# Kernel tuning notes

Hardware: AMD Instinct MI355X
Metric: run time of the kernel (lower is better)

The kernel has to match this reference:

```python
import jax, jax.numpy as jnp
import numpy as np

EPS = 1e-7
N_INST = 16  # instance ids 1..16 (id 0 = background); all present w.h.p. given input distribution


def setup_inputs() -> dict:
    key = jax.random.key(0)
    k1, k2, k3 = jax.random.split(key, 3)
    pred_instance_mask = jax.random.uniform(k1, (4, 17, 768, 768), dtype=jnp.float32)
    cls_out = jax.random.uniform(k2, (4, 1, 768, 768), dtype=jnp.float32)
    target_mask = jax.random.randint(k3, (4, 1, 768, 768), 0, 17, dtype=jnp.int32)
    return {"pred_instance_mask": pred_instance_mask, "cls_out": cls_out, "target_mask": target_mask}


def _bce_dice(p, t):
    # BCEDiceLoss(activation=None): mean BCE on probabilities + soft-dice loss
    pc = jnp.clip(p, EPS, 1.0 - EPS)
    bce = -jnp.mean(t * jnp.log(pc) + (1.0 - t) * jnp.log1p(-pc))
    inter = jnp.sum(p * t)
    dice = 1.0 - (2.0 * inter + EPS) / (jnp.sum(p) + jnp.sum(t) + EPS)
    return bce + dice


def reference(pred_instance_mask, cls_out, target_mask):
    B, K, H, W = pred_instance_mask.shape
    tfg = (target_mask > 0).astype(jnp.float32)
    res = _bce_dice(cls_out, tfg)
    res = res + _bce_dice(pred_instance_mask[:, 0:1], 1.0 - tfg)

    # ---- pairwise BCEDice loss matrix L[n, k] for ids n=1..N_INST, channels k=1..K-1 ----
    # Each pairwise loss is over the FULL tensor (all B*H*W pixels), target = (target_mask == n).
    Pm = pred_instance_mask[:, 1:].transpose(1, 0, 2, 3).reshape(K - 1, -1)  # [K-1, M]
    Mpix = Pm.shape[1]
    tm = target_mask.reshape(-1)  # [M] int ids
    pc = jnp.clip(Pm, EPS, 1.0 - EPS)
    log1mp = jnp.log1p(-pc)
    D = log1mp - jnp.log(pc)  # [K-1, M]; BCE = mean(-log1mp) + mean(t * D)
    A = -jnp.mean(log1mp, axis=1)  # [K-1]
    segD = jax.ops.segment_sum(D.T, tm, num_segments=N_INST + 1)[1:]   # [N, K-1]
    segP = jax.ops.segment_sum(Pm.T, tm, num_segments=N_INST + 1)[1:]  # [N, K-1] = inter
    cnt = jax.ops.segment_sum(jnp.ones_like(tm, dtype=jnp.float32), tm, num_segments=N_INST + 1)[1:]  # [N]
    sum_p = jnp.sum(Pm, axis=1)  # [K-1]
    bce = A[None, :] + segD / jnp.float32(Mpix)
    dice = 1.0 - (2.0 * segP + EPS) / (sum_p[None, :] + cnt[:, None] + EPS)
    L = bce + dice  # [N, K-1]

    # ---- greedy assignment: ids in ascending order each grab the remaining best channel ----
    def step(carry, Ln):
        avail, total = carry
        masked = jnp.where(avail, Ln, jnp.inf)
        k = jnp.argmin(masked)
        return (avail.at[k].set(False), total + masked[k]), None

    (_, total), _ = jax.lax.scan(step, (jnp.ones(K - 1, dtype=bool), jnp.float32(0.0)), L)
    return (res + total) / N_INST
```

## Files before the change

### kernel.cpp

```cpp
#include <hip/hip_runtime.h>
#include <hip/hip_bf16.h>

#define HWPX 589824
#define MPIX 2359296
#define EPSF 1e-7f
#define LN2F 0.6931471805599453f
#define TILES 9
#define PXB  2304
#define NBLK 1024


typedef __attribute__((ext_vector_type(8))) short bf16x8;
typedef __attribute__((ext_vector_type(4))) float f32x4;

__device__ __forceinline__ short bfc(float x) {
    union { __hip_bfloat16 h; short s; } u;
    u.h = __float2bfloat16(x);
    return u.s;
}

__device__ __forceinline__ float wave_sum64(float v) {
#pragma unroll
    for (int o = 32; o; o >>= 1) v += __shfl_xor(v, o, 64);
    return v;
}

#define GLD16(gsrc, ldst) __builtin_amdgcn_global_load_lds( \
    (const __attribute__((address_space(1))) void*)(gsrc),  \
    (__attribute__((address_space(3))) void*)(ldst), 16, 0, 0)

#define WAITV(n) asm volatile("s_waitcnt vmcnt(" #n ")" ::: "memory")

__global__ __launch_bounds__(512, 8) void loss_main(
    const float* __restrict__ pred, const float* __restrict__ cls,
    const int* __restrict__ tm, float* __restrict__ acc)
{
    __shared__ float stage[2][16][256];
    __shared__ int   tmt[2][256];
    __shared__ float gD[256], gP[256];
    __shared__ float sCh[3][16][8];
    __shared__ float sC6[6][8];

    const int tid  = threadIdx.x;
    const int w    = tid >> 6;
    const int lane = tid & 63;
    const int g    = lane >> 4;
    const int q    = lane & 15;

    const long base = (long)blockIdx.x * PXB;
    const int b   = (int)(base / HWPX);
    const int off = (int)(base % HWPX);

    const int* trow = tm + (long)b * HWPX + off;
    const float* pbase17 = pred + (long)b * 17 * (long)HWPX + off;

    if (tid < 256) { gD[tid] = 0.f; gP[tid] = 0.f; }

#define STAGE(t_, buf_) do {                                                      \
        const int _r0 = w, _r1 = w + 8;                                           \
        GLD16(pbase17 + (long)(1 + _r0) * HWPX + (t_) * 256 + ((lane ^ (_r0 & 7)) << 2), \
              &stage[buf_][_r0][0]);                                              \
        GLD16(pbase17 + (long)(1 + _r1) * HWPX + (t_) * 256 + ((lane ^ (_r1 & 7)) << 2), \
              &stage[buf_][_r1][0]);                                              \
        if (w == 0) GLD16(trow + (t_) * 256 + (lane << 2), &tmt[buf_][0]);        \
    } while (0)

    STAGE(0, 0);

    f32x4 aD = {0.f, 0.f, 0.f, 0.f};
    f32x4 aP = {0.f, 0.f, 0.f, 0.f};
    float sl2 = 0.f, sp = 0.f, cf = 0.f;
    const int tgt = q + 1;
    const int s4 = w * 8 + g * 2;
    const int k8 = q & 7;

#pragma unroll 1
    for (int t = 0; t < TILES; ++t) {
        const int bi = t & 1;
        if (t + 1 < TILES) {
            STAGE(t + 1, bi ^ 1);
            if (w == 0) WAITV(3); else WAITV(2);
        } else {
            WAITV(0);
        }
        __syncthreads();

        const float4 pa = ((const float4*)&stage[bi][q][0])[s4 ^ k8];
        const float4 pb = ((const float4*)&stage[bi][q][0])[(s4 + 1) ^ k8];
        const int4   ta = ((const int4*)&tmt[bi][0])[s4];
        const int4   tb = ((const int4*)&tmt[bi][0])[s4 + 1];

        const float pv[8] = {pa.x,pa.y,pa.z,pa.w,pb.x,pb.y,pb.z,pb.w};
        const int   tv[8] = {ta.x,ta.y,ta.z,ta.w,tb.x,tb.y,tb.z,tb.w};
        bf16x8 av, bD, bP;
#pragma unroll
        for (int j = 0; j < 8; ++j) {
            const float p  = pv[j];
            const float pc = fminf(fmaxf(p, EPSF), 1.0f - EPSF);
            const float l2p  = __log2f(pc);
            const float l21p = __log2f(1.0f - pc);
            sl2 += l21p;
            sp  += p;
            bD[j] = bfc(l21p - l2p);
            bP[j] = bfc(p);
            const bool m = (tv[j] == tgt);
            av[j] = m ? (short)0x3F80 : (short)0;
            cf += m ? 1.f : 0.f;
        }
        aD = __builtin_amdgcn_mfma_f32_16x16x32_bf16(av, bD, aD, 0, 0, 0);
        aP = __builtin_amdgcn_mfma_f32_16x16x32_bf16(av, bP, aP, 0, 0, 0);
        __syncthreads();
    }
#undef STAGE

    sl2 += __shfl_xor(sl2, 16, 64); sl2 += __shfl_xor(sl2, 32, 64);
    sp  += __shfl_xor(sp,  16, 64); sp  += __shfl_xor(sp,  32, 64);
    cf  += __shfl_xor(cf,  16, 64); cf  += __shfl_xor(cf,  32, 64);
    if (lane < 16) { sCh[0][q][w] = sl2; sCh[1][q][w] = sp; sCh[2][q][w] = cf; }

#pragma unroll
    for (int r = 0; r < 4; ++r) {
        const int n = ((lane >> 4) << 2) + r;
        atomicAdd(&gD[n * 16 + q], aD[r]);
        atomicAdd(&gP[n * 16 + q], aP[r]);
    }

    const float* crow = cls + (long)b * HWPX + off;
    const float* zrow = pbase17;
    float s0c=0.f,s1c=0.f,s2c=0.f, s00=0.f,s10=0.f,s20=0.f;
    const int nch = (tid < 64) ? 2 : 1;
    for (int chunk = 0; chunk < nch; ++chunk) {
        const int pb2 = (chunk == 0) ? tid * 4 : 2048 + tid * 4;
        const float4 ca = *(const float4*)(crow + pb2);
        const float4 za = *(const float4*)(zrow + pb2);
        const int4   ua = *(const int4*)(trow + pb2);
        const float cv[4] = {ca.x,ca.y,ca.z,ca.w};
        const float zv[4] = {za.x,za.y,za.z,za.w};
        const int   uv[4] = {ua.x,ua.y,ua.z,ua.w};
#pragma unroll
        for (int j = 0; j < 4; ++j) {
            const int t = uv[j];
            { const float p = cv[j];
              const float pc = fminf(fmaxf(p, EPSF), 1.0f - EPSF);
              const float lp = __log2f(pc), l1p = __log2f(1.0f - pc);
              const bool fg = (t > 0);
              s0c += fg ? lp : l1p; s1c += fg ? p : 0.f; s2c += p; }
            { const float p = zv[j];
              const float pc = fminf(fmaxf(p, EPSF), 1.0f - EPSF);
              const float lp = __log2f(pc), l1p = __log2f(1.0f - pc);
              const bool bg = (t == 0);
              s00 += bg ? lp : l1p; s10 += bg ? p : 0.f; s20 += p; }
        }
    }
    s0c = wave_sum64(s0c); s1c = wave_sum64(s1c); s2c = wave_sum64(s2c);
    s00 = wave_sum64(s00); s10 = wave_sum64(s10); s20 = wave_sum64(s20);
    if (lane == 0) {
        sC6[0][w]=s0c; sC6[1][w]=s1c; sC6[2][w]=s2c;
        sC6[3][w]=s00; sC6[4][w]=s10; sC6[5][w]=s20;
    }
    __syncthreads();

    if (tid < 256) {
        atomicAdd(&acc[38 + tid], gD[tid]);
        atomicAdd(&acc[294 + tid], gP[tid]);
    } else if (tid < 304) {
        const int i = tid - 256, qq = i >> 4, ii = i & 15;
        float t = 0.f;
#pragma unroll
        for (int ww = 0; ww < 8; ++ww) t += sCh[qq][ii][ww];
        atomicAdd(&acc[(qq == 0) ? (6 + ii) : (qq == 1) ? (22 + ii) : (550 + ii)], t);
    } else if (tid < 310) {
        const int i = tid - 304;
        float t = 0.f;
#pragma unroll
        for (int ww = 0; ww < 8; ++ww) t += sC6[i][ww];
        atomicAdd(&acc[i], t);
    }
}

__global__ void loss_final(const float* __restrict__ acc, float* __restrict__ out)
{
    __shared__ float L[16][16];
    __shared__ float s_fg;
    const int tid = threadIdx.x;
    const float Mf = (float)MPIX;

    if (tid == 0) {
        float s = 0.f;
        for (int n = 0; n < 16; ++n) s += acc[550 + n];
        s_fg = s;
    }
    __syncthreads();

    if (tid < 256) {
        const int n = tid >> 4, k = tid & 15;
        const float segD = acc[38 + n * 16 + k];
        const float segP = acc[294 + n * 16 + k];
        const float sump = acc[22 + k];
        const float cn   = acc[550 + n];
        const float bce  = (segD - acc[6 + k]) * LN2F / Mf;
        const float dice = 1.f - (2.f * segP + EPSF) / (sump + cn + EPSF);
        L[n][k] = bce + dice;
    }
    __syncthreads();

    if (tid < 64) {
        const bool mine = (tid < 16);
        float total = 0.f;
        unsigned avail = mine ? 1u : 0u;
        for (int step = 0; step < 16; ++step) {
            float v = (mine && avail) ? L[step][tid] : 1e30f;
            int idx = tid;
            #pragma unroll
            for (int o = 8; o; o >>= 1) {
                const float ov = __shfl_xor(v, o, 64);
                const int   oi = __shfl_xor(idx, o, 64);
                if (ov < v || (ov == v && oi < idx)) { v = ov; idx = oi; }
            }
            if (tid == 0) total += v;
            if (tid == idx) avail = 0;
        }
        if (tid == 0) {
            const float cnt0 = Mf - s_fg;
            const float bce_c  = -acc[0] * LN2F / Mf;
            const float dice_c = 1.f - (2.f * acc[1] + EPSF) / (acc[2] + s_fg + EPSF);
            const float bce_0  = -acc[3] * LN2F / Mf;
            const float dice_0 = 1.f - (2.f * acc[4] + EPSF) / (acc[5] + cnt0 + EPSF);
            const float res = bce_c + dice_c + bce_0 + dice_0;
            out[0] = (res + total) / 16.f;
        }
    }
}

extern "C" void kernel_launch(void* const* d_in, const int* in_sizes, int n_in,
                              void* d_out, int out_size, void* d_ws, size_t ws_size,
                              hipStream_t stream)
{
    const float* pred = (const float*)d_in[0];
    const float* cls  = (const float*)d_in[1];
    const int*   tmi  = (const int*)d_in[2];
    float* acc = (float*)d_ws;

    hipMemsetAsync(d_ws, 0, 566 * sizeof(float), stream);

    loss_main<<<dim3(NBLK), 512, 0, stream>>>(pred, cls, tmi, acc);
    loss_final<<<1, 256, 0, stream>>>(acc, (float*)d_out);
}
```

Measured before the change: 80.84 us.

## Restructure main loss kernel: register-prefetched tiles, bf16 LDS staging, fewer bigger blocks

Drops the global_load_lds async staging of raw fp32 tiles. Each wave now prefetches its two channels' next 1024-pixel tile into registers with inline-asm dwordx4 loads while the current tile's MFMAs run. The loaded values are converted to log-diff and probability bf16 values once per channel, not once per (target, pixel) lane. Blocks grow to 9216 pixels, the grid shrinks to 256, and block order is swizzled. Channel sums are reduced per wave and written straight to global atomics. This removes redundant log evaluations, since the old layout recomputed the same logs in every q lane group, at the cost of more LDS footprint, lower occupancy and a full vmcnt drain each tile.

```diff
diff --git a/kernel.cpp b/kernel.cpp
--- a/kernel.cpp
+++ b/kernel.cpp
@@ -5,9 +5,10 @@
 #define MPIX 2359296
 #define EPSF 1e-7f
 #define LN2F 0.6931471805599453f
-#define TILES 9
-#define PXB  2304
-#define NBLK 1024
+#define TILE 1024
+#define NT   9
+#define BLKPX 9216
+#define NBLK 256
 
 
 typedef __attribute__((ext_vector_type(8))) short bf16x8;
@@ -25,20 +26,23 @@
     return v;
 }
 
-#define GLD16(gsrc, ldst) __builtin_amdgcn_global_load_lds( \
-    (const __attribute__((address_space(1))) void*)(gsrc),  \
-    (__attribute__((address_space(3))) void*)(ldst), 16, 0, 0)
-
-#define WAITV(n) asm volatile("s_waitcnt vmcnt(" #n ")" ::: "memory")
-
-__global__ __launch_bounds__(512, 8) void loss_main(
+#define ALOADF4(dst, addr) \
+    asm volatile("global_load_dwordx4 %0, %1, off" : "=&v"(dst) : "v"(addr) : "memory")
+#define ALOADI4(dst, addr) \
+    asm volatile("global_load_dwordx4 %0, %1, off" : "=&v"(dst) : "v"(addr) : "memory")
+#define VMDRAIN do { \
+    asm volatile("s_waitcnt vmcnt(0)" ::: "memory"); \
+    __builtin_amdgcn_sched_barrier(0); } while (0)
+
+__global__ __launch_bounds__(512) void loss_main(
     const float* __restrict__ pred, const float* __restrict__ cls,
     const int* __restrict__ tm, float* __restrict__ acc)
 {
-    __shared__ float stage[2][16][256];
-    __shared__ int   tmt[2][256];
+    __shared__ __attribute__((aligned(16))) short Dst[2][16][1032];
+    __shared__ __attribute__((aligned(16))) short Pst[2][16][1032];
+    __shared__ __attribute__((aligned(16))) int   tmt[2][1024];
     __shared__ float gD[256], gP[256];
-    __shared__ float sCh[3][16][8];
+    __shared__ float sCnt[16][8];
     __shared__ float sC6[6][8];
 
     const int tid  = threadIdx.x;
@@ -47,90 +51,121 @@
     const int g    = lane >> 4;
     const int q    = lane & 15;
 
-    const long base = (long)blockIdx.x * PXB;
-    const int b   = (int)(base / HWPX);
-    const int off = (int)(base % HWPX);
-
-    const int* trow = tm + (long)b * HWPX + off;
+    const int r   = ((blockIdx.x & 7) << 5) + (blockIdx.x >> 3);
+    const int b   = r >> 6;
+    const int off = (r & 63) * BLKPX;
+
+    const int*   trow    = tm + (long)b * HWPX + off;
     const float* pbase17 = pred + (long)b * 17 * (long)HWPX + off;
+    const int k0 = w, k1 = w + 8;
+    const float* prow0 = pbase17 + (long)(1 + k0) * HWPX;
+    const float* prow1 = pbase17 + (long)(1 + k1) * HWPX;
 
     if (tid < 256) { gD[tid] = 0.f; gP[tid] = 0.f; }
 
-#define STAGE(t_, buf_) do {                                                      \
-        const int _r0 = w, _r1 = w + 8;                                           \
-        GLD16(pbase17 + (long)(1 + _r0) * HWPX + (t_) * 256 + ((lane ^ (_r0 & 7)) << 2), \
-              &stage[buf_][_r0][0]);                                              \
-        GLD16(pbase17 + (long)(1 + _r1) * HWPX + (t_) * 256 + ((lane ^ (_r1 & 7)) << 2), \
-              &stage[buf_][_r1][0]);                                              \
-        if (w == 0) GLD16(trow + (t_) * 256 + (lane << 2), &tmt[buf_][0]);        \
-    } while (0)
-
-    STAGE(0, 0);
-
-    f32x4 aD = {0.f, 0.f, 0.f, 0.f};
-    f32x4 aP = {0.f, 0.f, 0.f, 0.f};
-    float sl2 = 0.f, sp = 0.f, cf = 0.f;
+    float4 L[8];  int4 T[4];
+#define ISSUE(ts) do { const int t0 = (ts) * TILE;                         \
+        ALOADF4(L[0], prow0 + t0 + lane * 8);                              \
+        ALOADF4(L[1], prow0 + t0 + lane * 8 + 4);                          \
+        ALOADF4(L[2], prow0 + t0 + 512 + lane * 8);                        \
+        ALOADF4(L[3], prow0 + t0 + 512 + lane * 8 + 4);                    \
+        ALOADF4(L[4], prow1 + t0 + lane * 8);                              \
+        ALOADF4(L[5], prow1 + t0 + lane * 8 + 4);                          \
+        ALOADF4(L[6], prow1 + t0 + 512 + lane * 8);                        \
+        ALOADF4(L[7], prow1 + t0 + 512 + lane * 8 + 4);                    \
+        if (w == 0) { _Pragma("unroll")                                    \
+            for (int j = 0; j < 4; ++j)                                    \
+                ALOADI4(T[j], trow + t0 + j * 256 + lane * 4); } } while (0)
+
+    float sl2_0 = 0.f, sp_0 = 0.f, sl2_1 = 0.f, sp_1 = 0.f;
+
+#define CVT8(u, v, ROW, H, SL, SP, buf) do {                               \
+        bf16x8 dd, pp;                                                     \
+        const float pvv[8] = {u.x,u.y,u.z,u.w,v.x,v.y,v.z,v.w};            \
+        _Pragma("unroll")                                                  \
+        for (int j = 0; j < 8; ++j) {                                      \
+            const float p = pvv[j];                                        \
+            const float pc = fminf(fmaxf(p, EPSF), 1.0f - EPSF);           \
+            const float l2p = __log2f(pc), l21p = __log2f(1.0f - pc);      \
+            SL += l21p; SP += p;                                           \
+            dd[j] = bfc(l21p - l2p); pp[j] = bfc(p);                       \
+        }                                                                  \
+        *(bf16x8*)&Dst[buf][ROW][(H) * 512 + lane * 8] = dd;               \
+        *(bf16x8*)&Pst[buf][ROW][(H) * 512 + lane * 8] = pp; } while (0)
+
+#define WRITE_TILE(buf) do {                                               \
+        CVT8(L[0], L[1], k0, 0, sl2_0, sp_0, buf);                         \
+        CVT8(L[2], L[3], k0, 1, sl2_0, sp_0, buf);                         \
+        CVT8(L[4], L[5], k1, 0, sl2_1, sp_1, buf);                         \
+        CVT8(L[6], L[7], k1, 1, sl2_1, sp_1, buf);                         \
+        if (w == 0) { _Pragma("unroll")                                    \
+            for (int j = 0; j < 4; ++j)                                    \
+                *(int4*)&tmt[buf][j * 256 + lane * 4] = T[j]; } } while (0)
+
+    ISSUE(0);
+    VMDRAIN;
+    WRITE_TILE(0);
+    __syncthreads();
+
+    f32x4 aD = {0.f,0.f,0.f,0.f}, aP = {0.f,0.f,0.f,0.f};
+    float cf = 0.f;
     const int tgt = q + 1;
-    const int s4 = w * 8 + g * 2;
-    const int k8 = q & 7;
 
 #pragma unroll 1
-    for (int t = 0; t < TILES; ++t) {
+    for (int t = 0; t < NT; ++t) {
         const int bi = t & 1;
-        if (t + 1 < TILES) {
-            STAGE(t + 1, bi ^ 1);
-            if (w == 0) WAITV(3); else WAITV(2);
-        } else {
-            WAITV(0);
+        if (t + 1 < NT) ISSUE(t + 1);
+#pragma unroll
+        for (int ks = 0; ks < 4; ++ks) {
+            const int px0 = w * 128 + ks * 32 + g * 8;
+            const bf16x8 dv = *(const bf16x8*)&Dst[bi][q][px0];
+            const bf16x8 pv = *(const bf16x8*)&Pst[bi][q][px0];
+            const int4 ta = *(const int4*)&tmt[bi][px0];
+            const int4 tb = *(const int4*)&tmt[bi][px0 + 4];
+            const int tv[8] = {ta.x,ta.y,ta.z,ta.w,tb.x,tb.y,tb.z,tb.w};
+            bf16x8 av;
+#pragma unroll
+            for (int j = 0; j < 8; ++j) {
+                const bool m = (tv[j] == tgt);
+                av[j] = m ? (short)0x3F80 : (short)0;
+                cf += m ? 1.f : 0.f;
+            }
+            aD = __builtin_amdgcn_mfma_f32_16x16x32_bf16(av, dv, aD, 0, 0, 0);
+            aP = __builtin_amdgcn_mfma_f32_16x16x32_bf16(av, pv, aP, 0, 0, 0);
+        }
+        if (t + 1 < NT) {
+            VMDRAIN;
+            WRITE_TILE(bi ^ 1);
         }
         __syncthreads();
-
-        const float4 pa = ((const float4*)&stage[bi][q][0])[s4 ^ k8];
-        const float4 pb = ((const float4*)&stage[bi][q][0])[(s4 + 1) ^ k8];
-        const int4   ta = ((const int4*)&tmt[bi][0])[s4];
-        const int4   tb = ((const int4*)&tmt[bi][0])[s4 + 1];
-
-        const float pv[8] = {pa.x,pa.y,pa.z,pa.w,pb.x,pb.y,pb.z,pb.w};
-        const int   tv[8] = {ta.x,ta.y,ta.z,ta.w,tb.x,tb.y,tb.z,tb.w};
-        bf16x8 av, bD, bP;
-#pragma unroll
-        for (int j = 0; j < 8; ++j) {
-            const float p  = pv[j];
-            const float pc = fminf(fmaxf(p, EPSF), 1.0f - EPSF);
-            const float l2p  = __log2f(pc);
-            const float l21p = __log2f(1.0f - pc);
-            sl2 += l21p;
-            sp  += p;
-            bD[j] = bfc(l21p - l2p);
-            bP[j] = bfc(p);
-            const bool m = (tv[j] == tgt);
-            av[j] = m ? (short)0x3F80 : (short)0;
-            cf += m ? 1.f : 0.f;
-        }
-        aD = __builtin_amdgcn_mfma_f32_16x16x32_bf16(av, bD, aD, 0, 0, 0);
-        aP = __builtin_amdgcn_mfma_f32_16x16x32_bf16(av, bP, aP, 0, 0, 0);
-        __syncthreads();
-    }
-#undef STAGE
-
-    sl2 += __shfl_xor(sl2, 16, 64); sl2 += __shfl_xor(sl2, 32, 64);
-    sp  += __shfl_xor(sp,  16, 64); sp  += __shfl_xor(sp,  32, 64);
-    cf  += __shfl_xor(cf,  16, 64); cf  += __shfl_xor(cf,  32, 64);
-    if (lane < 16) { sCh[0][q][w] = sl2; sCh[1][q][w] = sp; sCh[2][q][w] = cf; }
-
-#pragma unroll
-    for (int r = 0; r < 4; ++r) {
-        const int n = ((lane >> 4) << 2) + r;
-        atomicAdd(&gD[n * 16 + q], aD[r]);
-        atomicAdd(&gP[n * 16 + q], aP[r]);
+    }
+#undef ISSUE
+#undef WRITE_TILE
+#undef CVT8
+
+    sl2_0 = wave_sum64(sl2_0); sp_0 = wave_sum64(sp_0);
+    sl2_1 = wave_sum64(sl2_1); sp_1 = wave_sum64(sp_1);
+    if (lane == 0) {
+        atomicAdd(&acc[6 + k0], sl2_0);  atomicAdd(&acc[22 + k0], sp_0);
+        atomicAdd(&acc[6 + k1], sl2_1);  atomicAdd(&acc[22 + k1], sp_1);
+    }
+    cf += __shfl_xor(cf, 16, 64); cf += __shfl_xor(cf, 32, 64);
+    if (lane < 16) sCnt[q][w] = cf;
+
+#pragma unroll
+    for (int r_ = 0; r_ < 4; ++r_) {
+        const int n = ((lane >> 4) << 2) + r_;
+        atomicAdd(&gD[n * 16 + q], aD[r_]);
+        atomicAdd(&gP[n * 16 + q], aP[r_]);
     }
 
     const float* crow = cls + (long)b * HWPX + off;
     const float* zrow = pbase17;
     float s0c=0.f,s1c=0.f,s2c=0.f, s00=0.f,s10=0.f,s20=0.f;
-    const int nch = (tid < 64) ? 2 : 1;
-    for (int chunk = 0; chunk < nch; ++chunk) {
-        const int pb2 = (chunk == 0) ? tid * 4 : 2048 + tid * 4;
+#pragma unroll 1
+    for (int c = 0; c < 5; ++c) {
+        if (c == 4 && tid >= 256) break;
+        const int pb2 = c * 2048 + tid * 4;
         const float4 ca = *(const float4*)(crow + pb2);
         const float4 za = *(const float4*)(zrow + pb2);
         const int4   ua = *(const int4*)(trow + pb2);
@@ -163,14 +198,14 @@
     if (tid < 256) {
         atomicAdd(&acc[38 + tid], gD[tid]);
         atomicAdd(&acc[294 + tid], gP[tid]);
-    } else if (tid < 304) {
-        const int i = tid - 256, qq = i >> 4, ii = i & 15;
+    } else if (tid < 272) {
+        const int i = tid - 256;
         float t = 0.f;
 #pragma unroll
-        for (int ww = 0; ww < 8; ++ww) t += sCh[qq][ii][ww];
-        atomicAdd(&acc[(qq == 0) ? (6 + ii) : (qq == 1) ? (22 + ii) : (550 + ii)], t);
-    } else if (tid < 310) {
-        const int i = tid - 304;
+        for (int ww = 0; ww < 8; ++ww) t += sCnt[i][ww];
+        atomicAdd(&acc[550 + i], t);
+    } else if (tid < 278) {
+        const int i = tid - 272;
         float t = 0.f;
 #pragma unroll
         for (int ww = 0; ww < 8; ++ww) t += sC6[i][ww];
```

Result: slower. 109.8 us (+35.8%).
